# Optimization experiments

Hardware: AMD Instinct MI355X
Metric: run time of the kernel (lower is better)

Reference implementation:

```python
import jax, jax.numpy as jnp
import numpy as np

WS = (2, 6, 12)          # window (Wz, Wh, Ww)
SHIFT = (1, 3, 6)        # Wz//2, Wh//2, Ww//2
NUM_HEADS = 8
DIM = 256
HIDDEN = 1024            # mlp_ratio * dim
TYPE_OF_WINDOWS = 64     # (Z//Wz)*(H//Wh)
EPS = 1e-5


def _build_position_index(ws):
    Wz, Wh, Ww = ws
    zi = np.arange(Wz); zj = -np.arange(Wz) * Wz
    hi = np.arange(Wh); hj = -np.arange(Wh) * Wh
    w = np.arange(Ww)
    gzi, ghi, gw = np.meshgrid(zi, hi, w, indexing='ij')
    gzj, ghj, _ = np.meshgrid(zj, hj, w, indexing='ij')
    fi = np.stack([gzi.ravel(), ghi.ravel(), gw.ravel()])
    fj = np.stack([gzj.ravel(), ghj.ravel(), gw.ravel()])
    coords = fi[:, :, None] - fj[:, None, :]
    coords[2] += Ww - 1
    coords[1] *= 2 * Ww - 1
    coords[0] *= (2 * Ww - 1) * Wh * Wh
    return coords.sum(0).reshape(-1)  # (N*N,) int


def _window_partition(x, ws):
    # (B, Z, H, W, C) -> (B*n_windows, Wz*Wh*Ww, C)
    B, Z, H, W, C = x.shape
    Wz, Wh, Ww = ws
    x = x.reshape(B, Z // Wz, Wz, H // Wh, Wh, W // Ww, Ww, C)
    x = x.transpose(0, 1, 3, 5, 2, 4, 6, 7)
    return x.reshape(-1, Wz * Wh * Ww, C)


def _window_reverse(win, ws, B, Z, H, W):
    Wz, Wh, Ww = ws
    x = win.reshape(B, Z // Wz, H // Wh, W // Ww, Wz, Wh, Ww, -1)
    x = x.transpose(0, 1, 4, 2, 5, 3, 6, 7)
    return x.reshape(B, Z, H, W, -1)


def _build_shift_mask(Z, H, W, ws, shift):
    Wz, Wh, Ww = ws
    sz, sh, sw = shift
    img = np.zeros((1, Z, H, W, 1), dtype=np.float32)
    z_slices = (slice(0, -Wz), slice(-Wz, -sz), slice(-sz, None))
    h_slices = (slice(0, -Wh), slice(-Wh, -sh), slice(-sh, None))
    w_slices = (slice(0, -Ww), slice(-Ww, -sw), slice(-sw, None))
    cnt = 0
    for zs in z_slices:
        for hs in h_slices:
            for wsl in w_slices:
                img[:, zs, hs, wsl, :] = cnt
                cnt += 1
    m = _window_partition(img, ws)[..., 0]             # (n_w, N)
    am = m[:, None, :] - m[:, :, None]                 # (n_w, N, N)
    am = np.where(am != 0, -100.0, 0.0).astype(np.float32)
    return am[:, None]                                 # (n_w, 1, N, N)


def _ln(x, g, b):
    mu = x.mean(-1, keepdims=True)
    var = ((x - mu) ** 2).mean(-1, keepdims=True)
    return (x - mu) * jax.lax.rsqrt(var + EPS) * g + b


def setup_inputs() -> dict:
    key = jax.random.key(0)
    ks = jax.random.split(key, 16)
    B, Z, H, W, C = 1, 8, 96, 192, DIM
    n_unique = (2 * WS[2] - 1) * WS[1] * WS[1] * WS[0] * WS[0]  # 3312
    s = 0.02
    return {
        'x': jax.random.normal(ks[0], (B, Z * H * W, C), jnp.float32),
        'g1': jnp.ones((C,), jnp.float32),
        'beta1': jnp.zeros((C,), jnp.float32),
        'wqkv': jax.random.normal(ks[1], (3 * C, C), jnp.float32) * s,
        'bqkv': jnp.zeros((3 * C,), jnp.float32),
        'bias_table': jax.random.normal(ks[2], (n_unique, TYPE_OF_WINDOWS, NUM_HEADS), jnp.float32) * s,
        'wproj': jax.random.normal(ks[3], (C, C), jnp.float32) * s,
        'bproj': jnp.zeros((C,), jnp.float32),
        'g2': jnp.ones((C,), jnp.float32),
        'beta2': jnp.zeros((C,), jnp.float32),
        'w1': jax.random.normal(ks[4], (HIDDEN, C), jnp.float32) * s,
        'b1': jnp.zeros((HIDDEN,), jnp.float32),
        'w2': jax.random.normal(ks[5], (C, HIDDEN), jnp.float32) * s,
        'b2': jnp.zeros((C,), jnp.float32),
        'Z': Z, 'H': H, 'W': W, 'window_type_index': 0,
    }


def reference(x, g1, beta1, wqkv, bqkv, bias_table, wproj, bproj, g2, beta2,
              w1, b1, w2, b2, Z, H, W, window_type_index):
    B, L, C = x.shape
    hd = C // NUM_HEADS
    scale = hd ** (-0.5)
    N = WS[0] * WS[1] * WS[2]

    xs = _ln(x, g1, beta1).reshape(B, Z, H, W, C)
    # shift
    xs = jnp.roll(xs, (-SHIFT[0], -SHIFT[1], -SHIFT[2]), axis=(1, 2, 3))
    mask = jnp.asarray(_build_shift_mask(Z, H, W, WS, SHIFT))  # (n_w,1,N,N)

    win = _window_partition(xs, WS)                    # (Bw, N, C)
    Bw = win.shape[0]
    qkv = (win @ wqkv.T + bqkv).reshape(Bw, N, 3, NUM_HEADS, hd).transpose(2, 0, 3, 1, 4)
    q, k, v = qkv[0], qkv[1], qkv[2]                   # (Bw, h, N, hd)

    attn = jnp.einsum('bhnd,bhmd->bhnm', q * scale, k)
    pos_index = _build_position_index(WS)              # (N*N,)
    bias = bias_table[pos_index, window_type_index]    # (N*N, heads)
    bias = bias.reshape(N, N, NUM_HEADS).transpose(2, 0, 1)[None]
    attn = attn + bias

    n_w = mask.shape[0]
    attn = attn.reshape(B, n_w, NUM_HEADS, N, N) + mask[None]
    attn = jax.nn.softmax(attn, axis=-1).reshape(Bw, NUM_HEADS, N, N)

    out = jnp.einsum('bhnm,bhmd->bhnd', attn, v).transpose(0, 2, 1, 3).reshape(Bw, N, C)
    out = out @ wproj.T + bproj

    xr = _window_reverse(out, WS, B, Z, H, W)
    xr = jnp.roll(xr, SHIFT, axis=(1, 2, 3)).reshape(B, Z * H * W, C)

    x = x + xr
    h = _ln(x, g2, beta2)
    h = jax.nn.gelu(h @ w1.T + b1, approximate=False)
    h = h @ w2.T + b2
    return x + h
```

## Files before the change

### kernel.cpp

```cpp
#include <hip/hip_runtime.h>
#include <hip/hip_bf16.h>
#include <math.h>

#define L_TOK   147456
#define CDIM    256
#define C3      768
#define HID     1024
#define NWIN    1024
#define NTOK    144
#define NHEADS  8
#define HD      32
#define SCALE   0.1767766952966369f

typedef __attribute__((ext_vector_type(8))) short bfrag;
typedef __attribute__((ext_vector_type(4))) float f32x4;

__device__ __forceinline__ ushort f2bf(float f) {
    __hip_bfloat16 h = __float2bfloat16(f);
    return *reinterpret_cast<ushort*>(&h);
}
__device__ __forceinline__ float bf2f(ushort u) {
    __hip_bfloat16 h = *reinterpret_cast<__hip_bfloat16*>(&u);
    return __bfloat162float(h);
}

__device__ __forceinline__ void gld16(const ushort* g, ushort* l) {
    __builtin_amdgcn_global_load_lds(
        (const __attribute__((address_space(1))) void*)g,
        (__attribute__((address_space(3))) void*)l, 16, 0, 0);
}

__device__ __forceinline__ int shift_src(int gt) {
    const int win = gt / NTOK;
    const int nt  = gt - win * NTOK;
    const int wz = win >> 8, wh = (win >> 4) & 15, ww = win & 15;
    const int lz = nt / 72;
    const int t2 = nt - lz * 72;
    const int lh = t2 / 12, lw = t2 - lh * 12;
    const int z = (wz * 2 + lz + 1) & 7;
    int h = wh * 6 + lh + 3;  if (h >= 96)  h -= 96;
    int w = ww * 12 + lw + 6; if (w >= 192) w -= 192;
    return (z * 96 + h) * 192 + w;
}

__global__ __launch_bounds__(256) void stats_kernel(const float* __restrict__ x,
                                                    float* __restrict__ st)
{
    const int wave = threadIdx.x >> 6;
    const int lane = threadIdx.x & 63;
    const int row = blockIdx.x * 4 + wave;
    const float4 v = *(const float4*)(x + (size_t)row * CDIM + lane * 4);
    float s  = v.x + v.y + v.z + v.w;
    float ss = v.x*v.x + v.y*v.y + v.z*v.z + v.w*v.w;
    #pragma unroll
    for (int off = 32; off; off >>= 1) {
        s  += __shfl_xor(s,  off);
        ss += __shfl_xor(ss, off);
    }
    if (lane == 0) {
        const float mean = s * (1.0f / CDIM);
        const float var  = ss * (1.0f / CDIM) - mean * mean;
        st[row * 2 + 0] = mean;
        st[row * 2 + 1] = rsqrtf(var + 1e-5f);
    }
}

__global__ __launch_bounds__(256) void cvt_kernel(const float* __restrict__ s,
                                                  ushort* __restrict__ d)
{
    const int i = (blockIdx.x * 256 + threadIdx.x) * 4;
    const float4 v = *(const float4*)(s + i);
    d[i + 0] = f2bf(v.x); d[i + 1] = f2bf(v.y);
    d[i + 2] = f2bf(v.z); d[i + 3] = f2bf(v.w);
}

__global__ __launch_bounds__(256) void comb_pre_kernel(const float* __restrict__ bt,
                                                       const int* __restrict__ wti_p,
                                                       ushort* __restrict__ comb)
{
    const int e = blockIdx.x * 256 + threadIdx.x;
    const int wti = *wti_p;
    const int reg  = e & 3;
    const int lane = (e >> 2) & 63;
    const int t    = e >> 8;
    const int ct = t % 9;
    const int rb = (t / 9) % 9;
    const int h  = (t / 81) % 8;
    const int cls = t / 648;
    const int i = rb * 16 + ((lane >> 4) << 2) + reg;
    const int j = ct * 16 + (lane & 15);
    const int zi = i / 72, ri = i - zi * 72, hi = ri / 12, wi = ri - (ri / 12) * 12;
    const int zj = j / 72, rj = j - zj * 72, hj = rj / 12, wj = rj - (rj / 12) * 12;
    const int idx = (zi + 2 * zj) * 828 + (hi + 6 * hj) * 23 + (wi - wj + 11);
    const float bias = bt[((size_t)idx * 64 + wti) * 8 + h];
    const int cz = (cls >> 2) & 1, ch = (cls >> 1) & 1, cw = cls & 1;
    const int ri_ = (cz ? (zi == 0 ? 1 : 2) : 0) * 9
                  + (ch ? (hi < 3 ? 1 : 2) : 0) * 3
                  + (cw ? (wi < 6 ? 1 : 2) : 0);
    const int rj_ = (cz ? (zj == 0 ? 1 : 2) : 0) * 9
                  + (ch ? (hj < 3 ? 1 : 2) : 0) * 3
                  + (cw ? (wj < 6 ? 1 : 2) : 0);
    comb[e] = f2bf(bias + ((ri_ == rj_) ? 0.0f : -100.0f));
}

__global__ __launch_bounds__(64) void attn_kernel(const ushort* __restrict__ qkv,
                                                  const ushort* __restrict__ comb,
                                                  ushort* __restrict__ outb,
                                                  int win0)
{
    __shared__ ushort vt[32][168];
    __shared__ ushort pt[16][168];

    const int winl = blockIdx.x >> 3;
    const int head = blockIdx.x & 7;
    const int win  = win0 + winl;
    const int lane = threadIdx.x;
    const int g = lane >> 4, c = lane & 15;
    const int cls = (((win >> 8) == 3) ? 4 : 0)
                  | ((((win >> 4) & 15) == 15) ? 2 : 0)
                  | (((win & 15) == 15) ? 1 : 0);

    const ushort* qb = qkv + (((size_t)(winl * 3 + 0) * 8 + head) * NTOK) * HD;
    const ushort* kb = qkv + (((size_t)(winl * 3 + 1) * 8 + head) * NTOK) * HD;
    const ushort* vb = qkv + (((size_t)(winl * 3 + 2) * 8 + head) * NTOK) * HD;

    for (int i = lane; i < 512; i += 64) vt[i >> 4][144 + (i & 15)] = 0;
    for (int i = lane; i < 256; i += 64) pt[i >> 4][144 + (i & 15)] = 0;
    for (int base = lane * 8; base < NTOK * HD; base += 512) {
        const int j = base >> 5, d0 = base & 31;
        union { ushort u[8]; uint4 q; } tv;
        tv.q = *(const uint4*)(vb + base);
        #pragma unroll
        for (int e = 0; e < 8; ++e) vt[d0 + e][j] = tv.u[e];
    }
    __syncthreads();

    bfrag kf[9];
    #pragma unroll
    for (int ct = 0; ct < 9; ++ct)
        kf[ct] = *(const bfrag*)(kb + (size_t)(ct * 16 + c) * HD + g * 8);
    bfrag vf[2][5];
    #pragma unroll
    for (int nt = 0; nt < 2; ++nt)
        #pragma unroll
        for (int kt = 0; kt < 5; ++kt)
            vf[nt][kt] = *(const bfrag*)&vt[nt * 16 + c][kt * 32 + g * 8];

    const ushort* cb = comb + ((size_t)cls * 8 + head) * 81 * 256;

    for (int rb = 0; rb < 9; ++rb) {
        const bfrag aq = *(const bfrag*)(qb + (size_t)(rb * 16 + c) * HD + g * 8);
        f32x4 s[9];
        #pragma unroll
        for (int ct = 0; ct < 9; ++ct)
            s[ct] = __builtin_amdgcn_mfma_f32_16x16x32_bf16(
                aq, kf[ct], (f32x4){0.0f, 0.0f, 0.0f, 0.0f}, 0, 0, 0);

        #pragma unroll
        for (int ct = 0; ct < 9; ++ct) {
            const uint2 bw = *(const uint2*)(cb + (size_t)(rb * 9 + ct) * 256 + lane * 4);
            s[ct][0] += bf2f((ushort)(bw.x & 0xffff));
            s[ct][1] += bf2f((ushort)(bw.x >> 16));
            s[ct][2] += bf2f((ushort)(bw.y & 0xffff));
            s[ct][3] += bf2f((ushort)(bw.y >> 16));
        }

        float mx[4] = {-1e30f, -1e30f, -1e30f, -1e30f};
        #pragma unroll
        for (int ct = 0; ct < 9; ++ct)
            #pragma unroll
            for (int r = 0; r < 4; ++r) mx[r] = fmaxf(mx[r], s[ct][r]);
        #pragma unroll
        for (int off = 1; off < 16; off <<= 1)
            #pragma unroll
            for (int r = 0; r < 4; ++r) mx[r] = fmaxf(mx[r], __shfl_xor(mx[r], off));
        float sm[4] = {0.0f, 0.0f, 0.0f, 0.0f};
        #pragma unroll
        for (int ct = 0; ct < 9; ++ct)
            #pragma unroll
            for (int r = 0; r < 4; ++r) {
                const float e = __expf(s[ct][r] - mx[r]);
                s[ct][r] = e; sm[r] += e;
            }
        #pragma unroll
        for (int off = 1; off < 16; off <<= 1)
            #pragma unroll
            for (int r = 0; r < 4; ++r) sm[r] += __shfl_xor(sm[r], off);
        float inv[4];
        #pragma unroll
        for (int r = 0; r < 4; ++r) inv[r] = 1.0f / sm[r];

        #pragma unroll
        for (int ct = 0; ct < 9; ++ct)
            #pragma unroll
            for (int r = 0; r < 4; ++r)
                pt[g * 4 + r][ct * 16 + c] = f2bf(s[ct][r]);

        f32x4 o[2] = {(f32x4){0,0,0,0}, (f32x4){0,0,0,0}};
        #pragma unroll
        for (int kt = 0; kt < 5; ++kt) {
            const bfrag pa = *(const bfrag*)&pt[c][kt * 32 + g * 8];
            o[0] = __builtin_amdgcn_mfma_f32_16x16x32_bf16(pa, vf[0][kt], o[0], 0, 0, 0);
            o[1] = __builtin_amdgcn_mfma_f32_16x16x32_bf16(pa, vf[1][kt], o[1], 0, 0, 0);
        }

        const size_t ob = ((size_t)winl * NTOK + rb * 16 + g * 4) * CDIM + head * HD;
        #pragma unroll
        for (int nt = 0; nt < 2; ++nt)
            #pragma unroll
            for (int r = 0; r < 4; ++r)
                outb[ob + (size_t)r * CDIM + nt * 16 + c] = f2bf(o[nt][r] * inv[r]);
    }
}

template<int ASRC, int EPI>
__global__ __launch_bounds__(256) void mgemm(const void* __restrict__ Ap,
                                             const ushort* __restrict__ Bw,
                                             const float* __restrict__ bias,
                                             void* __restrict__ outp,
                                             const float* __restrict__ resid,
                                             const float* __restrict__ st,
                                             const float* __restrict__ lng,
                                             const float* __restrict__ lnb,
                                             int K, int grow0)
{
    __shared__ __align__(16) ushort Asb[128 * 64];
    __shared__ __align__(16) ushort Bsb[128 * 64];

    const int tid = threadIdx.x;
    const int m0 = blockIdx.x * 128;
    const int n0 = blockIdx.y * 128;
    const int w = tid >> 6, lane = tid & 63;
    const int wm = w >> 1, wn = w & 1;
    const int fr = lane & 15, kg = lane >> 4;
    const int wbase = tid & 192;

    f32x4 acc[4][4];
    #pragma unroll
    for (int i = 0; i < 4; ++i)
        #pragma unroll
        for (int j = 0; j < 4; ++j)
            acc[i][j] = (f32x4){0.0f, 0.0f, 0.0f, 0.0f};

    int lrow[4], lsl[4];
    #pragma unroll
    for (int it = 0; it < 4; ++it) {
        const int s = it * 256 + tid;
        lrow[it] = s >> 3;
        lsl[it]  = ((s & 7) ^ (lrow[it] & 7)) * 8;
    }

    size_t boff[4];
    #pragma unroll
    for (int it = 0; it < 4; ++it) boff[it] = (size_t)(n0 + lrow[it]) * K;

    size_t aoff[4];
    size_t arow_off = 0;
    float mean = 0.0f, rstd = 0.0f;
    if constexpr (ASRC == 0) {
        #pragma unroll
        for (int it = 0; it < 4; ++it) aoff[it] = (size_t)(m0 + lrow[it]) * K;
    } else {
        const int row = tid >> 1;
        const int gr  = grow0 + m0 + row;
        const int src = shift_src(gr);
        arow_off = (size_t)src * CDIM;
        mean = st[src * 2 + 0];
        rstd = st[src * 2 + 1];
    }

    for (int kt = 0; kt < K; kt += 64) {
        if constexpr (ASRC == 0) {
            const ushort* A = (const ushort*)Ap;
            #pragma unroll
            for (int it = 0; it < 4; ++it)
                gld16(A + aoff[it] + kt + lsl[it], &Asb[(it * 256 + wbase) * 8]);
        } else {
            const float* A = (const float*)Ap;
            const int row = tid >> 1, half = tid & 1;
            #pragma unroll
            for (int q = 0; q < 4; ++q) {
                const int c = kt + half * 32 + q * 8;
                const float4 v0 = *(const float4*)(A + arow_off + c);
                const float4 v1 = *(const float4*)(A + arow_off + c + 4);
                const float4 g0 = *(const float4*)(lng + c);
                const float4 g1 = *(const float4*)(lng + c + 4);
                const float4 b0 = *(const float4*)(lnb + c);
                const float4 b1 = *(const float4*)(lnb + c + 4);
                union { ushort u[8]; uint4 q4; } pk;
                pk.u[0] = f2bf((v0.x - mean) * rstd * g0.x + b0.x);
                pk.u[1] = f2bf((v0.y - mean) * rstd * g0.y + b0.y);
                pk.u[2] = f2bf((v0.z - mean) * rstd * g0.z + b0.z);
                pk.u[3] = f2bf((v0.w - mean) * rstd * g0.w + b0.w);
                pk.u[4] = f2bf((v1.x - mean) * rstd * g1.x + b1.x);
                pk.u[5] = f2bf((v1.y - mean) * rstd * g1.y + b1.y);
                pk.u[6] = f2bf((v1.z - mean) * rstd * g1.z + b1.z);
                pk.u[7] = f2bf((v1.w - mean) * rstd * g1.w + b1.w);
                const int sl = (half * 4 + q) ^ (row & 7);
                *(uint4*)&Asb[row * 64 + sl * 8] = pk.q4;
            }
        }
        #pragma unroll
        for (int it = 0; it < 4; ++it)
            gld16(Bw + boff[it] + kt + lsl[it], &Bsb[(it * 256 + wbase) * 8]);
        __syncthreads();

        #pragma unroll
        for (int kh = 0; kh < 2; ++kh) {
            bfrag af[4], bfv[4];
            #pragma unroll
            for (int fm = 0; fm < 4; ++fm) {
                const int r = wm * 64 + fm * 16 + fr;
                af[fm] = *(const bfrag*)&Asb[r * 64 + (((kh * 4 + kg) ^ (r & 7)) * 8)];
            }
            #pragma unroll
            for (int fn = 0; fn < 4; ++fn) {
                const int r = wn * 64 + fn * 16 + fr;
                bfv[fn] = *(const bfrag*)&Bsb[r * 64 + (((kh * 4 + kg) ^ (r & 7)) * 8)];
            }
            #pragma unroll
            for (int fm = 0; fm < 4; ++fm)
                #pragma unroll
                for (int fn = 0; fn < 4; ++fn)
                    acc[fm][fn] = __builtin_amdgcn_mfma_f32_16x16x32_bf16(
                        af[fm], bfv[fn], acc[fm][fn], 0, 0, 0);
        }
        __syncthreads();
    }

    #pragma unroll
    for (int fn = 0; fn < 4; ++fn) {
        const int col = n0 + wn * 64 + fn * 16 + fr;
        const float bv = bias[col];
        #pragma unroll
        for (int fm = 0; fm < 4; ++fm) {
            #pragma unroll
            for (int r = 0; r < 4; ++r) {
                const int mi = m0 + wm * 64 + fm * 16 + kg * 4 + r;
                float val = acc[fm][fn][r] + bv;
                if constexpr (EPI == 0) {
                    if (col < 256) val *= SCALE;
                    const int winl = mi / NTOK, nt = mi - (mi / NTOK) * NTOK;
                    const int sel = col >> 8, head = (col >> 5) & 7, d = col & 31;
                    ((ushort*)outp)[(((size_t)(winl * 3 + sel) * 8 + head) * NTOK + nt) * HD + d] = f2bf(val);
                } else {
                    const int p = shift_src(grow0 + mi);
                    ((float*)outp)[(size_t)p * CDIM + col] = resid[(size_t)p * CDIM + col] + val;
                }
            }
        }
    }
}

__global__ __launch_bounds__(512) void mlp_fused(float* __restrict__ io,
                                                 const ushort* __restrict__ w1b,
                                                 const float* __restrict__ b1,
                                                 const ushort* __restrict__ w2b,
                                                 const float* __restrict__ b2,
                                                 const float* __restrict__ g2,
                                                 const float* __restrict__ beta2)
{
    __shared__ __align__(16) ushort lds[40960];
    ushort* XS = lds;
    ushort* HS = lds + 16384;
    ushort* SB = lds + 24576;

    const int tid = threadIdx.x;
    const int w = tid >> 6, lane = tid & 63;
    const int wm = w >> 2, wn = w & 3;
    const int fr = lane & 15, kg = lane >> 4;
    const int wbase = tid & 0x1C0;
    const int grow0 = blockIdx.x * 64;

    {
        const int row = tid >> 3;
        const int oct = tid & 7;
        const float* xr = io + (size_t)(grow0 + row) * CDIM + oct * 32;
        float4 v[8];
        float s = 0.0f, ss = 0.0f;
        #pragma unroll
        for (int j = 0; j < 8; ++j) {
            v[j] = *(const float4*)(xr + j * 4);
            s  += v[j].x + v[j].y + v[j].z + v[j].w;
            ss += v[j].x*v[j].x + v[j].y*v[j].y + v[j].z*v[j].z + v[j].w*v[j].w;
        }
        #pragma unroll
        for (int off = 1; off < 8; off <<= 1) {
            s  += __shfl_xor(s,  off);
            ss += __shfl_xor(ss, off);
        }
        const float mean = s * (1.0f / CDIM);
        const float var  = ss * (1.0f / CDIM) - mean * mean;
        const float rstd = rsqrtf(var + 1e-5f);
        #pragma unroll
        for (int j = 0; j < 4; ++j) {
            const int c = oct * 32 + j * 8;
            const float4 ga = *(const float4*)(g2 + c);
            const float4 gb = *(const float4*)(g2 + c + 4);
            const float4 ba = *(const float4*)(beta2 + c);
            const float4 bb = *(const float4*)(beta2 + c + 4);
            union { ushort u[8]; uint4 q4; } pk;
            pk.u[0] = f2bf((v[2*j].x   - mean) * rstd * ga.x + ba.x);
            pk.u[1] = f2bf((v[2*j].y   - mean) * rstd * ga.y + ba.y);
            pk.u[2] = f2bf((v[2*j].z   - mean) * rstd * ga.z + ba.z);
            pk.u[3] = f2bf((v[2*j].w   - mean) * rstd * ga.w + ba.w);
            pk.u[4] = f2bf((v[2*j+1].x - mean) * rstd * gb.x + bb.x);
            pk.u[5] = f2bf((v[2*j+1].y - mean) * rstd * gb.y + bb.y);
            pk.u[6] = f2bf((v[2*j+1].z - mean) * rstd * gb.z + bb.z);
            pk.u[7] = f2bf((v[2*j+1].w - mean) * rstd * gb.w + bb.w);
            const int slot = oct * 4 + j;
            *(uint4*)&XS[row * 256 + (slot ^ (row & 7)) * 8] = pk.q4;
        }
    }

    f32x4 acc[2][4];
    #pragma unroll
    for (int i = 0; i < 2; ++i)
        #pragma unroll
        for (int j = 0; j < 4; ++j)
            acc[i][j] = (f32x4){0.0f, 0.0f, 0.0f, 0.0f};

    for (int s = 0; s < 8; ++s) {
        f32x4 c1[2][2];
        #pragma unroll
        for (int i = 0; i < 2; ++i) { c1[i][0] = (f32x4){0,0,0,0}; c1[i][1] = (f32x4){0,0,0,0}; }
        for (int kt = 0; kt < 4; ++kt) {
            __syncthreads();
            #pragma unroll
            for (int i = 0; i < 2; ++i) {
                const int slot = i * 512 + tid;
                const int row = slot >> 3;
                const int sl = (slot & 7) ^ (row & 7);
                gld16(w1b + (size_t)(s * 128 + row) * 256 + kt * 64 + sl * 8,
                      &SB[(i * 512 + wbase) * 8]);
            }
            __syncthreads();
            #pragma unroll
            for (int ks = 0; ks < 2; ++ks) {
                bfrag af[2], bf2[2];
                #pragma unroll
                for (int fm = 0; fm < 2; ++fm) {
                    const int r = wm * 32 + fm * 16 + fr;
                    const int slot = kt * 8 + ks * 4 + kg;
                    af[fm] = *(const bfrag*)&XS[r * 256 + (slot ^ (r & 7)) * 8];
                }
                #pragma unroll
                for (int fn = 0; fn < 2; ++fn) {
                    const int r = wn * 32 + fn * 16 + fr;
                    const int slot = ks * 4 + kg;
                    bf2[fn] = *(const bfrag*)&SB[r * 64 + (slot ^ (r & 7)) * 8];
                }
                #pragma unroll
                for (int fm = 0; fm < 2; ++fm)
                    #pragma unroll
                    for (int fn = 0; fn < 2; ++fn)
                        c1[fm][fn] = __builtin_amdgcn_mfma_f32_16x16x32_bf16(
                            af[fm], bf2[fn], c1[fm][fn], 0, 0, 0);
            }
        }
        #pragma unroll
        for (int fn = 0; fn < 2; ++fn) {
            const int colh = wn * 32 + fn * 16 + fr;
            const float b1v = b1[s * 128 + colh];
            #pragma unroll
            for (int fm = 0; fm < 2; ++fm) {
                #pragma unroll
                for (int r = 0; r < 4; ++r) {
                    const int mi = wm * 32 + fm * 16 + kg * 4 + r;
                    const float v = c1[fm][fn][r] + b1v;
                    const float ge = 0.5f * v * (1.0f + erff(v * 0.70710678118654752f));
                    HS[mi * 128 + ((colh >> 3) ^ (mi & 7)) * 8 + (colh & 7)] = f2bf(ge);
                }
            }
        }
        for (int kt2 = 0; kt2 < 2; ++kt2) {
            __syncthreads();
            #pragma unroll
            for (int i = 0; i < 4; ++i) {
                const int slot = i * 512 + tid;
                const int row = slot >> 3;
                const int sl = (slot & 7) ^ (row & 7);
                gld16(w2b + (size_t)row * 1024 + s * 128 + kt2 * 64 + sl * 8,
                      &SB[(i * 512 + wbase) * 8]);
            }
            __syncthreads();
            #pragma unroll
            for (int ks = 0; ks < 2; ++ks) {
                bfrag af[2], bf4[4];
                #pragma unroll
                for (int fm = 0; fm < 2; ++fm) {
                    const int r = wm * 32 + fm * 16 + fr;
                    const int slot = kt2 * 8 + ks * 4 + kg;
                    af[fm] = *(const bfrag*)&HS[r * 128 + (slot ^ (r & 7)) * 8];
                }
                #pragma unroll
                for (int fn = 0; fn < 4; ++fn) {
                    const int r = wn * 64 + fn * 16 + fr;
                    const int slot = ks * 4 + kg;
                    bf4[fn] = *(const bfrag*)&SB[r * 64 + (slot ^ (r & 7)) * 8];
                }
                #pragma unroll
                for (int fm = 0; fm < 2; ++fm)
                    #pragma unroll
                    for (int fn = 0; fn < 4; ++fn)
                        acc[fm][fn] = __builtin_amdgcn_mfma_f32_16x16x32_bf16(
                            af[fm], bf4[fn], acc[fm][fn], 0, 0, 0);
            }
        }
    }

    #pragma unroll
    for (int fn = 0; fn < 4; ++fn) {
        const int col = wn * 64 + fn * 16 + fr;
        const float bv = b2[col];
        #pragma unroll
        for (int fm = 0; fm < 2; ++fm) {
            #pragma unroll
            for (int r = 0; r < 4; ++r) {
                const int mi = wm * 32 + fm * 16 + kg * 4 + r;
                const size_t gi = (size_t)(grow0 + mi) * CDIM + col;
                io[gi] += acc[fm][fn][r] + bv;
            }
        }
    }
}

extern "C" void kernel_launch(void* const* d_in, const int* in_sizes, int n_in,
                              void* d_out, int out_size, void* d_ws, size_t ws_size,
                              hipStream_t stream)
{
    const float* x     = (const float*)d_in[0];
    const float* g1    = (const float*)d_in[1];
    const float* beta1 = (const float*)d_in[2];
    const float* wqkv  = (const float*)d_in[3];
    const float* bqkv  = (const float*)d_in[4];
    const float* btab  = (const float*)d_in[5];
    const float* wproj = (const float*)d_in[6];
    const float* bproj = (const float*)d_in[7];
    const float* g2    = (const float*)d_in[8];
    const float* beta2 = (const float*)d_in[9];
    const float* w1    = (const float*)d_in[10];
    const float* b1    = (const float*)d_in[11];
    const float* w2    = (const float*)d_in[12];
    const float* b2    = (const float*)d_in[13];
    const int*   wti   = (const int*)d_in[17];
    float* out = (float*)d_out;

    const size_t COMB_ELEMS = (size_t)8 * 8 * 81 * 256;
    const size_t WQKV_E = (size_t)C3 * CDIM, WP_E = (size_t)CDIM * CDIM;
    const size_t W1_E = (size_t)HID * CDIM,  W2_E = (size_t)CDIM * HID;
    const size_t base_bytes = COMB_ELEMS * 2 + (size_t)L_TOK * 2 * 4
                            + (WQKV_E + WP_E + W1_E + W2_E) * 2;

    int nch = 32;
    for (int cand : {4, 8, 16, 32}) {
        const size_t rows = (size_t)L_TOK / cand;
        if (base_bytes + rows * (C3 + CDIM) * 2 <= ws_size) { nch = cand; break; }
    }
    const int wins_per = NWIN / nch;
    const int rows_per = wins_per * NTOK;

    char* wsp = (char*)d_ws;
    ushort* comb = (ushort*)wsp; wsp += COMB_ELEMS * 2;
    float* st1 = (float*)wsp;  wsp += (size_t)L_TOK * 2 * 4;
    ushort* wq_b = (ushort*)wsp; wsp += WQKV_E * 2;
    ushort* wp_b = (ushort*)wsp; wsp += WP_E * 2;
    ushort* w1_b = (ushort*)wsp; wsp += W1_E * 2;
    ushort* w2_b = (ushort*)wsp; wsp += W2_E * 2;
    ushort* ratt = (ushort*)wsp; wsp += (size_t)rows_per * CDIM * 2;
    ushort* rbig = (ushort*)wsp;

    cvt_kernel<<<(int)(WQKV_E / 1024), 256, 0, stream>>>(wqkv, wq_b);
    cvt_kernel<<<(int)(WP_E   / 1024), 256, 0, stream>>>(wproj, wp_b);
    cvt_kernel<<<(int)(W1_E   / 1024), 256, 0, stream>>>(w1, w1_b);
    cvt_kernel<<<(int)(W2_E   / 1024), 256, 0, stream>>>(w2, w2_b);
    comb_pre_kernel<<<(int)(COMB_ELEMS / 256), 256, 0, stream>>>(btab, wti, comb);
    stats_kernel<<<L_TOK / 4, 256, 0, stream>>>(x, st1);

    for (int c = 0; c < nch; ++c) {
        const int row0 = c * rows_per;
        const int win0 = c * wins_per;
        mgemm<1, 0><<<dim3(rows_per / 128, C3 / 128), 256, 0, stream>>>(
            x, wq_b, bqkv, rbig, nullptr, st1, g1, beta1, CDIM, row0);
        attn_kernel<<<wins_per * NHEADS, 64, 0, stream>>>(rbig, comb, ratt, win0);
        mgemm<0, 1><<<dim3(rows_per / 128, CDIM / 128), 256, 0, stream>>>(
            ratt, wp_b, bproj, out, x, nullptr, nullptr, nullptr, CDIM, row0);
    }

    mlp_fused<<<L_TOK / 64, 512, 0, stream>>>(out, w1_b, b1, w2_b, b2, g2, beta2);
}
```

Baseline: 894.1 us.

## Double-buffer MLP weight tiles with software-pipelined async loads

Restructures the fused MLP loop into a flat 64-step schedule. Each step's weight tile (W1 or W2) streams into one of two alternating LDS buffers while the previous tile is consumed, so global loads overlap the MFMA work instead of being fenced by paired __syncthreads. The W2 tiles are reshaped to 32-wide K chunks so every step loads the same amount. The GELU output is written to LDS as packed 32-bit pairs using a lane shuffle. This relies on hand-placed vmcnt waits and raw barriers, which adds synchronisation risk.

```diff
diff --git a/kernel.cpp b/kernel.cpp
--- a/kernel.cpp
+++ b/kernel.cpp
@@ -361,9 +361,10 @@
                                                  const float* __restrict__ beta2)
 {
     __shared__ __align__(16) ushort lds[40960];
-    ushort* XS = lds;
-    ushort* HS = lds + 16384;
-    ushort* SB = lds + 24576;
+    ushort* XS  = lds;
+    ushort* HS  = lds + 16384;
+    ushort* SB0 = lds + 24576;
+    ushort* SB1 = lds + 32768;
 
     const int tid = threadIdx.x;
     const int w = tid >> 6, lane = tid & 63;
@@ -412,6 +413,30 @@
             *(uint4*)&XS[row * 256 + (slot ^ (row & 7)) * 8] = pk.q4;
         }
     }
+    __syncthreads();
+
+    auto issue = [&](int tg) {
+        const int s = tg >> 3, t = tg & 7;
+        ushort* dst = (tg & 1) ? SB1 : SB0;
+        if (t < 4) {
+            #pragma unroll
+            for (int i = 0; i < 2; ++i) {
+                const int L = i * 512 + tid;
+                const int row = L >> 3, slot = L & 7;
+                gld16(w1b + (size_t)(s * 128 + row) * 256 + t * 64 + ((slot ^ (row & 7)) * 8),
+                      dst + (i * 512 + wbase) * 8);
+            }
+        } else {
+            const int u = t - 4;
+            #pragma unroll
+            for (int i = 0; i < 2; ++i) {
+                const int L = i * 512 + tid;
+                const int row = L >> 2, slot = L & 3;
+                gld16(w2b + (size_t)row * 1024 + s * 128 + u * 32 + ((slot ^ (row & 3)) * 8),
+                      dst + (i * 512 + wbase) * 8);
+            }
+        }
+    };
 
     f32x4 acc[2][4];
     #pragma unroll
@@ -419,94 +444,92 @@
         #pragma unroll
         for (int j = 0; j < 4; ++j)
             acc[i][j] = (f32x4){0.0f, 0.0f, 0.0f, 0.0f};
-
-    for (int s = 0; s < 8; ++s) {
-        f32x4 c1[2][2];
-        #pragma unroll
-        for (int i = 0; i < 2; ++i) { c1[i][0] = (f32x4){0,0,0,0}; c1[i][1] = (f32x4){0,0,0,0}; }
-        for (int kt = 0; kt < 4; ++kt) {
-            __syncthreads();
-            #pragma unroll
-            for (int i = 0; i < 2; ++i) {
-                const int slot = i * 512 + tid;
-                const int row = slot >> 3;
-                const int sl = (slot & 7) ^ (row & 7);
-                gld16(w1b + (size_t)(s * 128 + row) * 256 + kt * 64 + sl * 8,
-                      &SB[(i * 512 + wbase) * 8]);
-            }
-            __syncthreads();
+    f32x4 c1[2][2];
+
+    issue(0);
+    for (int tg = 0; tg < 64; ++tg) {
+        const int s = tg >> 3, t = tg & 7;
+        const ushort* SB = (tg & 1) ? SB1 : SB0;
+
+        if (tg < 63) {
+            issue(tg + 1);
+            asm volatile("s_waitcnt vmcnt(2)" ::: "memory");
+        } else {
+            asm volatile("s_waitcnt vmcnt(0)" ::: "memory");
+        }
+        __builtin_amdgcn_s_barrier();
+
+        if (t < 4) {
+            if (t == 0) {
+                #pragma unroll
+                for (int i = 0; i < 2; ++i) { c1[i][0] = (f32x4){0,0,0,0}; c1[i][1] = (f32x4){0,0,0,0}; }
+            }
             #pragma unroll
             for (int ks = 0; ks < 2; ++ks) {
-                bfrag af[2], bf2[2];
+                bfrag af[2], bw[2];
                 #pragma unroll
                 for (int fm = 0; fm < 2; ++fm) {
                     const int r = wm * 32 + fm * 16 + fr;
-                    const int slot = kt * 8 + ks * 4 + kg;
-                    af[fm] = *(const bfrag*)&XS[r * 256 + (slot ^ (r & 7)) * 8];
+                    const int slot = t * 8 + ks * 4 + kg;
+                    af[fm] = *(const bfrag*)&XS[r * 256 + ((slot ^ (r & 7)) * 8)];
                 }
                 #pragma unroll
                 for (int fn = 0; fn < 2; ++fn) {
                     const int r = wn * 32 + fn * 16 + fr;
                     const int slot = ks * 4 + kg;
-                    bf2[fn] = *(const bfrag*)&SB[r * 64 + (slot ^ (r & 7)) * 8];
+                    bw[fn] = *(const bfrag*)&SB[r * 64 + ((slot ^ (r & 7)) * 8)];
                 }
                 #pragma unroll
                 for (int fm = 0; fm < 2; ++fm)
                     #pragma unroll
                     for (int fn = 0; fn < 2; ++fn)
                         c1[fm][fn] = __builtin_amdgcn_mfma_f32_16x16x32_bf16(
-                            af[fm], bf2[fn], c1[fm][fn], 0, 0, 0);
-            }
-        }
-        #pragma unroll
-        for (int fn = 0; fn < 2; ++fn) {
-            const int colh = wn * 32 + fn * 16 + fr;
-            const float b1v = b1[s * 128 + colh];
+                            af[fm], bw[fn], c1[fm][fn], 0, 0, 0);
+            }
+            if (t == 3) {
+                #pragma unroll
+                for (int fn = 0; fn < 2; ++fn) {
+                    const int colh = wn * 32 + fn * 16 + fr;
+                    const float b1v = b1[s * 128 + colh];
+                    #pragma unroll
+                    for (int fm = 0; fm < 2; ++fm) {
+                        #pragma unroll
+                        for (int r = 0; r < 4; ++r) {
+                            const int mi = wm * 32 + fm * 16 + kg * 4 + r;
+                            const float v = c1[fm][fn][r] + b1v;
+                            const float ge = 0.5f * v * (1.0f + erff(v * 0.70710678118654752f));
+                            const int hv = f2bf(ge);
+                            const int ov = __shfl_xor(hv, 1);
+                            if ((fr & 1) == 0) {
+                                const int idx = mi * 128 + ((colh >> 3) ^ (mi & 7)) * 8 + (colh & 7);
+                                *(uint*)&HS[idx] = (uint)(hv & 0xffff) | ((uint)ov << 16);
+                            }
+                        }
+                    }
+                }
+                asm volatile("s_waitcnt lgkmcnt(0)" ::: "memory");
+            }
+        } else {
+            const int u = t - 4;
+            bfrag af[2], bw[4];
             #pragma unroll
             for (int fm = 0; fm < 2; ++fm) {
+                const int r = wm * 32 + fm * 16 + fr;
+                af[fm] = *(const bfrag*)&HS[r * 128 + (((u * 4 + kg) ^ (r & 7)) * 8)];
+            }
+            #pragma unroll
+            for (int fn = 0; fn < 4; ++fn) {
+                const int r = wn * 64 + fn * 16 + fr;
+                bw[fn] = *(const bfrag*)&SB[r * 32 + ((kg ^ (r & 3)) * 8)];
+            }
+            #pragma unroll
+            for (int fm = 0; fm < 2; ++fm)
                 #pragma unroll
-                for (int r = 0; r < 4; ++r) {
-                    const int mi = wm * 32 + fm * 16 + kg * 4 + r;
-                    const float v = c1[fm][fn][r] + b1v;
-                    const float ge = 0.5f * v * (1.0f + erff(v * 0.70710678118654752f));
-                    HS[mi * 128 + ((colh >> 3) ^ (mi & 7)) * 8 + (colh & 7)] = f2bf(ge);
-                }
-            }
-        }
-        for (int kt2 = 0; kt2 < 2; ++kt2) {
-            __syncthreads();
-            #pragma unroll
-            for (int i = 0; i < 4; ++i) {
-                const int slot = i * 512 + tid;
-                const int row = slot >> 3;
-                const int sl = (slot & 7) ^ (row & 7);
-                gld16(w2b + (size_t)row * 1024 + s * 128 + kt2 * 64 + sl * 8,
-                      &SB[(i * 512 + wbase) * 8]);
-            }
-            __syncthreads();
-            #pragma unroll
-            for (int ks = 0; ks < 2; ++ks) {
-                bfrag af[2], bf4[4];
-                #pragma unroll
-                for (int fm = 0; fm < 2; ++fm) {
-                    const int r = wm * 32 + fm * 16 + fr;
-                    const int slot = kt2 * 8 + ks * 4 + kg;
-                    af[fm] = *(const bfrag*)&HS[r * 128 + (slot ^ (r & 7)) * 8];
-                }
-                #pragma unroll
-                for (int fn = 0; fn < 4; ++fn) {
-                    const int r = wn * 64 + fn * 16 + fr;
-                    const int slot = ks * 4 + kg;
-                    bf4[fn] = *(const bfrag*)&SB[r * 64 + (slot ^ (r & 7)) * 8];
-                }
-                #pragma unroll
-                for (int fm = 0; fm < 2; ++fm)
-                    #pragma unroll
-                    for (int fn = 0; fn < 4; ++fn)
-                        acc[fm][fn] = __builtin_amdgcn_mfma_f32_16x16x32_bf16(
-                            af[fm], bf4[fn], acc[fm][fn], 0, 0, 0);
-            }
-        }
+                for (int fn = 0; fn < 4; ++fn)
+                    acc[fm][fn] = __builtin_amdgcn_mfma_f32_16x16x32_bf16(
+                        af[fm], bw[fn], acc[fm][fn], 0, 0, 0);
+        }
+        __builtin_amdgcn_s_barrier();
     }
 
     #pragma unroll
```

Result: slower. 1.094 ms (+22.4%).

## Precompute shifted LayerNorm1 into bf16 buffer and pack GELU LDS stores

Applied to the files above, without the earlier changes.

Replaces the separate stats pass and the in-GEMM fp32 LayerNorm A-load with a per-chunk ln1 kernel. That kernel gathers the shifted token rows, normalizes them and writes bf16 into the attention buffer. The QKV GEMM then loads A through the async global-to-LDS path, like the projection GEMM. Before, that GEMM repeated the fp32 loads and LN math for each of its 6 N-tiles. The cost is an extra bf16 write and read per chunk plus one more launch per chunk. Separately, the MLP's GELU stores to LDS are paired via a lane shuffle into 32-bit writes.

```diff
diff --git a/kernel.cpp b/kernel.cpp
--- a/kernel.cpp
+++ b/kernel.cpp
@@ -43,26 +43,35 @@
     return (z * 96 + h) * 192 + w;
 }
 
-__global__ __launch_bounds__(256) void stats_kernel(const float* __restrict__ x,
-                                                    float* __restrict__ st)
+__global__ __launch_bounds__(256) void ln1_kernel(const float* __restrict__ x,
+                                                  const float* __restrict__ g,
+                                                  const float* __restrict__ b,
+                                                  ushort* __restrict__ xw,
+                                                  int row0)
 {
     const int wave = threadIdx.x >> 6;
     const int lane = threadIdx.x & 63;
-    const int row = blockIdx.x * 4 + wave;
-    const float4 v = *(const float4*)(x + (size_t)row * CDIM + lane * 4);
-    float s  = v.x + v.y + v.z + v.w;
-    float ss = v.x*v.x + v.y*v.y + v.z*v.z + v.w*v.w;
+    const int t = blockIdx.x * 4 + wave;
+    const int src = shift_src(row0 + t);
+    const float4 xv = *(const float4*)(x + (size_t)src * CDIM + lane * 4);
+    float s  = xv.x + xv.y + xv.z + xv.w;
+    float ss = xv.x*xv.x + xv.y*xv.y + xv.z*xv.z + xv.w*xv.w;
     #pragma unroll
     for (int off = 32; off; off >>= 1) {
         s  += __shfl_xor(s,  off);
         ss += __shfl_xor(ss, off);
     }
-    if (lane == 0) {
-        const float mean = s * (1.0f / CDIM);
-        const float var  = ss * (1.0f / CDIM) - mean * mean;
-        st[row * 2 + 0] = mean;
-        st[row * 2 + 1] = rsqrtf(var + 1e-5f);
-    }
+    const float mean = s * (1.0f / CDIM);
+    const float var  = ss * (1.0f / CDIM) - mean * mean;
+    const float rstd = rsqrtf(var + 1e-5f);
+    const float4 gv = *(const float4*)(g + lane * 4);
+    const float4 bv = *(const float4*)(b + lane * 4);
+    union { ushort u[4]; uint2 q; } pk;
+    pk.u[0] = f2bf((xv.x - mean) * rstd * gv.x + bv.x);
+    pk.u[1] = f2bf((xv.y - mean) * rstd * gv.y + bv.y);
+    pk.u[2] = f2bf((xv.z - mean) * rstd * gv.z + bv.z);
+    pk.u[3] = f2bf((xv.w - mean) * rstd * gv.w + bv.w);
+    *(uint2*)(xw + (size_t)t * CDIM + lane * 4) = pk.q;
 }
 
 __global__ __launch_bounds__(256) void cvt_kernel(const float* __restrict__ s,
@@ -213,15 +222,12 @@
     }
 }
 
-template<int ASRC, int EPI>
-__global__ __launch_bounds__(256) void mgemm(const void* __restrict__ Ap,
+template<int EPI>
+__global__ __launch_bounds__(256) void mgemm(const ushort* __restrict__ A,
                                              const ushort* __restrict__ Bw,
                                              const float* __restrict__ bias,
                                              void* __restrict__ outp,
                                              const float* __restrict__ resid,
-                                             const float* __restrict__ st,
-                                             const float* __restrict__ lng,
-                                             const float* __restrict__ lnb,
                                              int K, int grow0)
 {
     __shared__ __align__(16) ushort Asb[128 * 64];
@@ -250,56 +256,17 @@
         lsl[it]  = ((s & 7) ^ (lrow[it] & 7)) * 8;
     }
 
-    size_t boff[4];
-    #pragma unroll
-    for (int it = 0; it < 4; ++it) boff[it] = (size_t)(n0 + lrow[it]) * K;
-
-    size_t aoff[4];
-    size_t arow_off = 0;
-    float mean = 0.0f, rstd = 0.0f;
-    if constexpr (ASRC == 0) {
-        #pragma unroll
-        for (int it = 0; it < 4; ++it) aoff[it] = (size_t)(m0 + lrow[it]) * K;
-    } else {
-        const int row = tid >> 1;
-        const int gr  = grow0 + m0 + row;
-        const int src = shift_src(gr);
-        arow_off = (size_t)src * CDIM;
-        mean = st[src * 2 + 0];
-        rstd = st[src * 2 + 1];
+    size_t aoff[4], boff[4];
+    #pragma unroll
+    for (int it = 0; it < 4; ++it) {
+        aoff[it] = (size_t)(m0 + lrow[it]) * K;
+        boff[it] = (size_t)(n0 + lrow[it]) * K;
     }
 
     for (int kt = 0; kt < K; kt += 64) {
-        if constexpr (ASRC == 0) {
-            const ushort* A = (const ushort*)Ap;
-            #pragma unroll
-            for (int it = 0; it < 4; ++it)
-                gld16(A + aoff[it] + kt + lsl[it], &Asb[(it * 256 + wbase) * 8]);
-        } else {
-            const float* A = (const float*)Ap;
-            const int row = tid >> 1, half = tid & 1;
-            #pragma unroll
-            for (int q = 0; q < 4; ++q) {
-                const int c = kt + half * 32 + q * 8;
-                const float4 v0 = *(const float4*)(A + arow_off + c);
-                const float4 v1 = *(const float4*)(A + arow_off + c + 4);
-                const float4 g0 = *(const float4*)(lng + c);
-                const float4 g1 = *(const float4*)(lng + c + 4);
-                const float4 b0 = *(const float4*)(lnb + c);
-                const float4 b1 = *(const float4*)(lnb + c + 4);
-                union { ushort u[8]; uint4 q4; } pk;
-                pk.u[0] = f2bf((v0.x - mean) * rstd * g0.x + b0.x);
-                pk.u[1] = f2bf((v0.y - mean) * rstd * g0.y + b0.y);
-                pk.u[2] = f2bf((v0.z - mean) * rstd * g0.z + b0.z);
-                pk.u[3] = f2bf((v0.w - mean) * rstd * g0.w + b0.w);
-                pk.u[4] = f2bf((v1.x - mean) * rstd * g1.x + b1.x);
-                pk.u[5] = f2bf((v1.y - mean) * rstd * g1.y + b1.y);
-                pk.u[6] = f2bf((v1.z - mean) * rstd * g1.z + b1.z);
-                pk.u[7] = f2bf((v1.w - mean) * rstd * g1.w + b1.w);
-                const int sl = (half * 4 + q) ^ (row & 7);
-                *(uint4*)&Asb[row * 64 + sl * 8] = pk.q4;
-            }
-        }
+        #pragma unroll
+        for (int it = 0; it < 4; ++it)
+            gld16(A + aoff[it] + kt + lsl[it], &Asb[(it * 256 + wbase) * 8]);
         #pragma unroll
         for (int it = 0; it < 4; ++it)
             gld16(Bw + boff[it] + kt + lsl[it], &Bsb[(it * 256 + wbase) * 8]);
@@ -469,7 +436,12 @@
                     const int mi = wm * 32 + fm * 16 + kg * 4 + r;
                     const float v = c1[fm][fn][r] + b1v;
                     const float ge = 0.5f * v * (1.0f + erff(v * 0.70710678118654752f));
-                    HS[mi * 128 + ((colh >> 3) ^ (mi & 7)) * 8 + (colh & 7)] = f2bf(ge);
+                    const int hv = f2bf(ge);
+                    const int ov = __shfl_xor(hv, 1);
+                    if ((fr & 1) == 0) {
+                        const int idx = mi * 128 + ((colh >> 3) ^ (mi & 7)) * 8 + (colh & 7);
+                        *(uint*)&HS[idx] = (uint)(hv & 0xffff) | ((uint)(ov & 0xffff) << 16);
+                    }
                 }
             }
         }
@@ -549,7 +521,7 @@
     const size_t COMB_ELEMS = (size_t)8 * 8 * 81 * 256;
     const size_t WQKV_E = (size_t)C3 * CDIM, WP_E = (size_t)CDIM * CDIM;
     const size_t W1_E = (size_t)HID * CDIM,  W2_E = (size_t)CDIM * HID;
-    const size_t base_bytes = COMB_ELEMS * 2 + (size_t)L_TOK * 2 * 4
+    const size_t base_bytes = COMB_ELEMS * 2
                             + (WQKV_E + WP_E + W1_E + W2_E) * 2;
 
     int nch = 32;
@@ -562,7 +534,6 @@
 
     char* wsp = (char*)d_ws;
     ushort* comb = (ushort*)wsp; wsp += COMB_ELEMS * 2;
-    float* st1 = (float*)wsp;  wsp += (size_t)L_TOK * 2 * 4;
     ushort* wq_b = (ushort*)wsp; wsp += WQKV_E * 2;
     ushort* wp_b = (ushort*)wsp; wsp += WP_E * 2;
     ushort* w1_b = (ushort*)wsp; wsp += W1_E * 2;
@@ -575,16 +546,16 @@
     cvt_kernel<<<(int)(W1_E   / 1024), 256, 0, stream>>>(w1, w1_b);
     cvt_kernel<<<(int)(W2_E   / 1024), 256, 0, stream>>>(w2, w2_b);
     comb_pre_kernel<<<(int)(COMB_ELEMS / 256), 256, 0, stream>>>(btab, wti, comb);
-    stats_kernel<<<L_TOK / 4, 256, 0, stream>>>(x, st1);
 
     for (int c = 0; c < nch; ++c) {
         const int row0 = c * rows_per;
         const int win0 = c * wins_per;
-        mgemm<1, 0><<<dim3(rows_per / 128, C3 / 128), 256, 0, stream>>>(
-            x, wq_b, bqkv, rbig, nullptr, st1, g1, beta1, CDIM, row0);
+        ln1_kernel<<<rows_per / 4, 256, 0, stream>>>(x, g1, beta1, ratt, row0);
+        mgemm<0><<<dim3(rows_per / 128, C3 / 128), 256, 0, stream>>>(
+            ratt, wq_b, bqkv, rbig, nullptr, CDIM, row0);
         attn_kernel<<<wins_per * NHEADS, 64, 0, stream>>>(rbig, comb, ratt, win0);
-        mgemm<0, 1><<<dim3(rows_per / 128, CDIM / 128), 256, 0, stream>>>(
-            ratt, wp_b, bproj, out, x, nullptr, nullptr, nullptr, CDIM, row0);
+        mgemm<1><<<dim3(rows_per / 128, CDIM / 128), 256, 0, stream>>>(
+            ratt, wp_b, bproj, out, x, CDIM, row0);
     }
 
     mlp_fused<<<L_TOK / 64, 512, 0, stream>>>(out, w1_b, b1, w2_b, b2, g2, beta2);
```

Result: faster. 766.5 us (-14.3%).
